# Optimization experiments

Hardware: AMD Instinct MI355X
Metric: run time of the kernel (lower is better)

## Reference

```python
import jax, jax.numpy as jnp
import numpy as np

B, P, C, H, W = 256, 512, 512, 7, 8
T = H * W  # 56
EPS = 1e-8


def setup_inputs() -> dict:
    key = jax.random.key(0)
    k1, k2, k3 = jax.random.split(key, 3)
    inp = jax.random.normal(k1, (B, C, H, W), dtype=jnp.float32)
    # xavier-uniform-like init for prototype (fan over last two dims as torch does)
    bound_p = float(np.sqrt(6.0 / (P + C * T)))
    prototype = jax.random.uniform(k2, (P, C, T), dtype=jnp.float32, minval=-bound_p, maxval=bound_p)
    bound_w = float(np.sqrt(6.0 / (C + 1)))
    fc_w = jax.random.uniform(k3, (1, C), dtype=jnp.float32, minval=-bound_w, maxval=bound_w)
    fc_b = jnp.zeros((1,), dtype=jnp.float32)
    return {"input": inp, "prototype": prototype, "fc_w": fc_w, "fc_b": fc_b}


def reference(input, prototype, fc_w, fc_b):
    # flatten spatial dims: (B, C, T)
    x = input.reshape(input.shape[0], input.shape[1], -1)
    # per-position cosine similarity over channel dim
    dots = jnp.einsum('bct,pct->bpt', x, prototype)          # (B, P, T)
    xn = jnp.linalg.norm(x, axis=1)                           # (B, T)
    pn = jnp.linalg.norm(prototype, axis=1)                   # (P, T)
    sim = dots / jnp.maximum(xn[:, None, :] * pn[None, :, :], EPS)
    att = jax.nn.softmax(sim, axis=-1)                        # (B, P, T)
    # attention-pooled elementwise product: (B, P, C)
    feat = jnp.einsum('bpt,bct,pct->bpc', att, x, prototype)
    # fc: Linear(C, 1) then relu, view to (B, P)
    out = jax.nn.relu(jnp.einsum('bpc,oc->bpo', feat, fc_w) + fc_b)
    return out.reshape(out.shape[0], out.shape[1])
```

## Files before the change

kernel.cpp:

```cpp
#include <hip/hip_runtime.h>
#include <hip/hip_bf16.h>
#include <math.h>

constexpr int kB = 256, kC = 512, kT = 56, kP = 512;
constexpr int kCT = kC * kT;

typedef short v4s __attribute__((ext_vector_type(4)));
typedef short v8s __attribute__((ext_vector_type(8)));
typedef float v4f __attribute__((ext_vector_type(4)));
typedef float v16f __attribute__((ext_vector_type(16)));

__device__ __forceinline__ unsigned pack_bf16(float a, float b) {
  __hip_bfloat16 ha = __float2bfloat16(a);
  __hip_bfloat16 hb = __float2bfloat16(b);
  unsigned short ua, ub;
  __builtin_memcpy(&ua, &ha, 2);
  __builtin_memcpy(&ub, &hb, 2);
  return (unsigned)ua | ((unsigned)ub << 16);
}

__device__ __forceinline__ v4s frag2(unsigned w0, unsigned w1) {
  unsigned u[2] = {w0, w1};
  v4s s;
  __builtin_memcpy(&s, u, 8);
  return s;
}

__device__ __forceinline__ v8s frag8(uint4 u) {
  v8s s;
  __builtin_memcpy(&s, &u, 16);
  return s;
}

__device__ __forceinline__ unsigned cvtpk(float lo, float hi) {
  unsigned r;
  asm("v_cvt_pk_bf16_f32 %0, %1, %2" : "=v"(r) : "v"(lo), "v"(hi));
  return r;
}

#define GLOAD(gp, lp)                                                        \
  __builtin_amdgcn_global_load_lds(                                          \
      (const __attribute__((address_space(1))) unsigned*)(const unsigned*)(gp), \
      (__attribute__((address_space(3))) unsigned*)(unsigned*)(lp), 16, 0, 0)

__global__ __launch_bounds__(512) void zero_kernel(float* __restrict__ p) {
  p[blockIdx.x * 512 + threadIdx.x] = 0.f;
}

__global__ __launch_bounds__(512) void prep_kernel(
    const float* __restrict__ x, const float* __restrict__ proto,
    const float* __restrict__ fcw,
    unsigned* __restrict__ xt, unsigned* __restrict__ xwt,
    unsigned* __restrict__ pt,
    float* __restrict__ xn2, float* __restrict__ pn2) {
  __shared__ float tile[128 * 64];
  __shared__ float normp[56 * 16];

  const int tid = threadIdx.x;
  const int bidx = blockIdx.x;
  const int n = bidx >> 2;
  const int ch = bidx & 3;
  const bool isx = (n < kB);
  const int row = isx ? n : (n - kB);
  const float* csrc = (isx ? x : proto) + (size_t)row * kCT + ch * (128 * 56);

  const int l = tid & 63;
  const int w = tid >> 6;
  const int j = l & 15;
  const int tq = l >> 4;

  float fw[8];
  if (isx) {
    const float* gf = fcw + ch * 128 + 8 * j;
#pragma unroll
    for (int i = 0; i < 8; ++i) fw[i] = gf[i];
  }

#pragma unroll
  for (int it = 0; it < 4; ++it) {
    const int idx = it * 512 + tid;
    if (idx < 1792) {
      const int f0 = idx * 4;
      const int c = (int)(((unsigned)f0 * 74899u) >> 22);
      const int t = f0 - c * 56;
      const int sw = ((((unsigned)c >> 3) ^ (unsigned)c) & 7) << 2;
      float4 v = *(const float4*)(csrc + f0);
      *(float4*)(tile + c * 64 + (t ^ sw)) = v;
    }
  }
  __syncthreads();

#pragma unroll
  for (int pass = 0; pass < 2; ++pass) {
    const int t = pass * 32 + w * 4 + tq;
    if (t < 56) {
      float f[8];
#pragma unroll
      for (int i = 0; i < 8; ++i) {
        const int sw = ((j ^ i) & 7) << 2;
        f[i] = tile[(8 * j + i) * 64 + (t ^ sw)];
      }
      float s = 0.f;
#pragma unroll
      for (int i = 0; i < 8; ++i) s = fmaf(f[i], f[i], s);
      normp[t * 16 + j] = s;
      uint4 wx;
      wx.x = cvtpk(f[0], f[1]);
      wx.y = cvtpk(f[2], f[3]);
      wx.z = cvtpk(f[4], f[5]);
      wx.w = cvtpk(f[6], f[7]);
      if (isx) {
        const size_t o = ((size_t)(t * kB + row)) * 256 + ch * 64 + 4 * j;
        *(uint4*)(xt + o) = wx;
        uint4 ww;
        ww.x = cvtpk(f[0] * fw[0], f[1] * fw[1]);
        ww.y = cvtpk(f[2] * fw[2], f[3] * fw[3]);
        ww.z = cvtpk(f[4] * fw[4], f[5] * fw[5]);
        ww.w = cvtpk(f[6] * fw[6], f[7] * fw[7]);
        *(uint4*)(xwt + o) = ww;
      } else {
        *(uint4*)(pt + ((size_t)(t * kP + row)) * 256 + ch * 64 + 4 * j) = wx;
      }
    }
  }
  __syncthreads();

  if (tid < 56) {
    float s = 0.f;
#pragma unroll
    for (int k = 0; k < 16; ++k) s += normp[tid * 16 + k];
    if (isx) atomicAdd(&xn2[row * 56 + tid], s);
    else     atomicAdd(&pn2[row * 56 + tid], s);
  }
}

constexpr int TILE = 64 * 32;
constexpr int BUF = 3 * TILE;

__global__ __launch_bounds__(256, 2) void proto_gemm_kernel(
    const unsigned* __restrict__ xt, const unsigned* __restrict__ xwt,
    const unsigned* __restrict__ pt,
    const float* __restrict__ xn2, const float* __restrict__ pn2,
    float* __restrict__ part) {
  __shared__ __align__(16) unsigned lds[3 * BUF];
  __shared__ float xnL[4 * 64], pnL[4 * 64];

  const int tid = threadIdx.x;
  const int l = tid & 63;
  const int w4 = tid >> 6;
  const int wm = w4 >> 1;
  const int wn = w4 & 1;

  int bid = (int)blockIdx.x;
  bid = (bid & 7) * 56 + (bid >> 3);
  const int b0 = (bid & 3) * 64;
  const int p0 = ((bid >> 2) & 7) * 64;
  const int tg = bid >> 5;

  {
    const int tl = tid >> 6, r = tid & 63;
    xnL[tid] = sqrtf(xn2[(b0 + r) * 56 + tg * 4 + tl]);
    pnL[tid] = sqrtf(pn2[(p0 + r) * 56 + tg * 4 + tl]);
  }
  __syncthreads();

  const int lrow = l >> 3, lch = l & 7;
  size_t xsrc[2], psrc[2];
  int ldst[2];
#pragma unroll
  for (int j = 0; j < 2; ++j) {
    const int row = w4 * 16 + j * 8 + lrow;
    const int ch4 = ((lch ^ (row & 7))) * 4;
    xsrc[j] = (size_t)(b0 + row) * 256 + ch4;
    psrc[j] = (size_t)(p0 + row) * 256 + ch4;
    ldst[j] = (w4 * 16 + j * 8) * 32;
  }

  const int fr = l & 31;
  const int hi = l >> 5;
  const int axb = (wm * 32 + fr) * 32;
  const int pxb = (wn * 32 + fr) * 32;
  const int frs = fr & 7;

  v16f aD, aW, sac, nac;
#pragma unroll
  for (int i = 0; i < 16; ++i) { aD[i] = 0.f; aW[i] = 0.f; sac[i] = 0.f; nac[i] = 0.f; }

  auto STAGE = [&](int s, int buf) {
    const int t = tg * 4 + (s >> 3);
    const size_t xo = (size_t)t * (kB * 256) + (size_t)((s & 7) * 32);
    const size_t po = (size_t)t * (kP * 256) + (size_t)((s & 7) * 32);
    unsigned* lb = lds + buf * BUF;
#pragma unroll
    for (int j = 0; j < 2; ++j) {
      GLOAD(xt + xsrc[j] + xo, lb + ldst[j]);
      GLOAD(xwt + xsrc[j] + xo, lb + TILE + ldst[j]);
      GLOAD(pt + psrc[j] + po, lb + 2 * TILE + ldst[j]);
    }
  };

  auto COMPUTE = [&](int s, int buf) {
    const unsigned* bx = lds + buf * BUF;
#pragma unroll
    for (int ks = 0; ks < 4; ++ks) {
      const int col = (((ks << 1) | hi) ^ frs) << 2;
      v8s xf = frag8(*(const uint4*)(bx + axb + col));
      v8s wf = frag8(*(const uint4*)(bx + TILE + axb + col));
      v8s pf = frag8(*(const uint4*)(bx + 2 * TILE + pxb + col));
      aD = __builtin_amdgcn_mfma_f32_32x32x16_bf16(xf, pf, aD, 0, 0, 0);
      aW = __builtin_amdgcn_mfma_f32_32x32x16_bf16(wf, pf, aW, 0, 0, 0);
    }
    if ((s & 7) == 7) {
      const int tl = s >> 3;
      const float pnv = pnL[tl * 64 + wn * 32 + fr];
#pragma unroll
      for (int i = 0; i < 16; ++i) {
        const int drow = (i & 3) + 8 * (i >> 2) + 4 * hi;
        const float xnv = xnL[tl * 64 + wm * 32 + drow];
        float den = fmaxf(xnv * pnv, 1e-8f);
        float sim = aD[i] * __builtin_amdgcn_rcpf(den);
        float e = __expf(sim);
        sac[i] += e;
        nac[i] = fmaf(e, aW[i], nac[i]);
        aD[i] = 0.f;
        aW[i] = 0.f;
      }
    }
  };

  STAGE(0, 0);
  STAGE(1, 1);

  int c0 = 0, c1 = 1, c2 = 2;
#pragma unroll 1
  for (int s = 0; s < 32; ++s) {
    if (s < 31) asm volatile("s_waitcnt vmcnt(6)" ::: "memory");
    else        asm volatile("s_waitcnt vmcnt(0)" ::: "memory");
    __builtin_amdgcn_s_barrier();
    __builtin_amdgcn_sched_barrier(0);
    COMPUTE(s, c0);
    if (s < 30) STAGE(s + 2, c2);
    const int tmp = c0; c0 = c1; c1 = c2; c2 = tmp;
  }

  float* psb = part + ((size_t)tg * 2 + 0) * 131072;
  float* pnb = part + ((size_t)tg * 2 + 1) * 131072;
#pragma unroll
  for (int i = 0; i < 16; ++i) {
    const int drow = (i & 3) + 8 * (i >> 2) + 4 * hi;
    const size_t o = (size_t)(b0 + wm * 32 + drow) * 512 + p0 + wn * 32 + fr;
    psb[o] = sac[i];
    pnb[o] = nac[i];
  }
}

__global__ __launch_bounds__(256) void merge_kernel(
    const float* __restrict__ part, const float* __restrict__ fcb,
    float* __restrict__ out) {
  const int pair = blockIdx.x * 256 + threadIdx.x;
  float S = 0.f, N = 0.f;
#pragma unroll
  for (int k = 0; k < 14; ++k) {
    S += part[((size_t)k * 2 + 0) * 131072 + pair];
    N += part[((size_t)k * 2 + 1) * 131072 + pair];
  }
  float o = N * __builtin_amdgcn_rcpf(S) + fcb[0];
  out[pair] = fmaxf(o, 0.f);
}

__global__ __launch_bounds__(1024) void proto_mfma_kernel(
    const float* __restrict__ x, const float* __restrict__ proto,
    const float* __restrict__ fcw, const float* __restrict__ fcb,
    float* __restrict__ out) {
  __shared__ unsigned xs[56 * 289];
  __shared__ unsigned ps[56 * 145];
  __shared__ unsigned pws[56 * 145];

  const int tid = threadIdx.x;
  const int l = tid & 63;
  const int w = tid >> 6;
  const int bq = w & 1;
  const int tq = w >> 1;
  const int t0 = tq * 7;

  const int n = blockIdx.y * 32 + blockIdx.x;
  const int p0 = (n >> 3) * 16;
  const int b0 = (n & 7) * 32;

  const bool act = (l < 56);
  const int lt = l;

  const int xbase0 = ((b0 + 2 * w + 0) * kC) * kT + lt;
  const int xbase1 = ((b0 + 2 * w + 1) * kC) * kT + lt;
  const int pbase = ((p0 + w) * kC) * kT + lt;

  const int arow = l & 15;
  const int q2 = (l >> 4) << 1;
  const int xoff = (bq * 16 + arow) * 9 + q2;
  const int poff = arow * 9 + q2;

  v4f acc[7][2];
#pragma unroll
  for (int ti = 0; ti < 7; ++ti) {
    acc[ti][0] = v4f{0.f, 0.f, 0.f, 0.f};
    acc[ti][1] = v4f{0.f, 0.f, 0.f, 0.f};
  }
  float xn2a = 0.f, xn2b = 0.f, pn2 = 0.f;

#pragma unroll 1
  for (int st = 0; st < 32; ++st) {
    const int k0 = st * 16;
    if (act) {
#pragma unroll
      for (int r = 0; r < 16; ++r) {
        const int cw = r & 7;
        const int c = k0 + 2 * cw;
        const int ga = ((r >> 3) ? xbase1 : xbase0) + c * kT;
        float g0 = x[ga], g1 = x[ga + kT];
        if (r >> 3) xn2b = fmaf(g0, g0, fmaf(g1, g1, xn2b));
        else xn2a = fmaf(g0, g0, fmaf(g1, g1, xn2a));
        xs[lt * 289 + (2 * w + (r >> 3)) * 9 + cw] = pack_bf16(g0, g1);
      }
#pragma unroll
      for (int cw = 0; cw < 8; ++cw) {
        const int c = k0 + 2 * cw;
        const int ga = pbase + c * kT;
        float g0 = proto[ga], g1 = proto[ga + kT];
        pn2 = fmaf(g0, g0, fmaf(g1, g1, pn2));
        ps[lt * 145 + w * 9 + cw] = pack_bf16(g0, g1);
        float f0 = fcw[c], f1 = fcw[c + 1];
        pws[lt * 145 + w * 9 + cw] = pack_bf16(g0 * f0, g1 * f1);
      }
    }
    __syncthreads();
#pragma unroll
    for (int ti = 0; ti < 7; ++ti) {
      const int t = t0 + ti;
      unsigned xw0 = xs[t * 289 + xoff];
      unsigned xw1 = xs[t * 289 + xoff + 1];
      unsigned pw0 = ps[t * 145 + poff];
      unsigned pw1 = ps[t * 145 + poff + 1];
      unsigned ww0 = pws[t * 145 + poff];
      unsigned ww1 = pws[t * 145 + poff + 1];
      v4s af = frag2(xw0, xw1);
      v4s bf = frag2(pw0, pw1);
      v4s wf = frag2(ww0, ww1);
      acc[ti][0] = __builtin_amdgcn_mfma_f32_16x16x16bf16_1k(af, bf, acc[ti][0], 0, 0, 0);
      acc[ti][1] = __builtin_amdgcn_mfma_f32_16x16x16bf16_1k(af, wf, acc[ti][1], 0, 0, 0);
    }
    __syncthreads();
  }

  float* xnorm = (float*)ps;
  float* pnorm = xnorm + 32 * 56;
  if (act) {
    xnorm[(2 * w + 0) * 56 + lt] = xn2a;
    xnorm[(2 * w + 1) * 56 + lt] = xn2b;
    pnorm[w * 56 + lt] = pn2;
  }
  __syncthreads();

  float* fm = (float*)xs;
  float* fsum = fm + 4096;
  float* fnum = fsum + 4096;
  const int pc = arow;
  const int qq = l >> 4;
#pragma unroll
  for (int i = 0; i < 4; ++i) {
    const int bl = bq * 16 + 4 * qq + i;
    float m = -3.0e38f;
    float sims[7];
#pragma unroll
    for (int ti = 0; ti < 7; ++ti) {
      const int t = t0 + ti;
      float den = fmaxf(sqrtf(xnorm[bl * 56 + t]) * sqrtf(pnorm[pc * 56 + t]), 1e-8f);
      float s = acc[ti][0][i] / den;
      sims[ti] = s;
      m = fmaxf(m, s);
    }
    float se = 0.f, nu = 0.f;
#pragma unroll
    for (int ti = 0; ti < 7; ++ti) {
      float e = __expf(sims[ti] - m);
      se += e;
      nu = fmaf(e, acc[ti][1][i], nu);
    }
    const int pair = bl * 16 + pc;
    fm[tq * 512 + pair] = m;
    fsum[tq * 512 + pair] = se;
    fnum[tq * 512 + pair] = nu;
  }
  __syncthreads();

  if (tid < 512) {
    float M = -3.0e38f;
#pragma unroll
    for (int k = 0; k < 8; ++k) M = fmaxf(M, fm[k * 512 + tid]);
    float S = 0.f, N = 0.f;
#pragma unroll
    for (int k = 0; k < 8; ++k) {
      float sc = __expf(fm[k * 512 + tid] - M);
      S = fmaf(fsum[k * 512 + tid], sc, S);
      N = fmaf(fnum[k * 512 + tid], sc, N);
    }
    float o = N / S + fcb[0];
    out[(b0 + (tid >> 4)) * kP + p0 + (tid & 15)] = fmaxf(o, 0.f);
  }
}

extern "C" void kernel_launch(void* const* d_in, const int* in_sizes, int n_in,
                              void* d_out, int out_size, void* d_ws, size_t ws_size,
                              hipStream_t stream) {
  const float* x = (const float*)d_in[0];
  const float* proto = (const float*)d_in[1];
  const float* fcw = (const float*)d_in[2];
  const float* fcb = (const float*)d_in[3];
  float* out = (float*)d_out;

  const size_t need = 73572352;
  if (ws_size >= need) {
    unsigned* xt = (unsigned*)d_ws;
    unsigned* xwt = xt + 3670016;
    unsigned* ptb = xt + 7340032;
    float* partb = (float*)(xt + 14680064);
    float* xn2b = (float*)(xt + 18350080);
    float* pn2b = xn2b + 14336;

    hipLaunchKernelGGL(zero_kernel, dim3(84), dim3(512), 0, stream, xn2b);

    hipLaunchKernelGGL(prep_kernel, dim3(4 * (kB + kP)), dim3(512), 0, stream,
                       x, proto, fcw, xt, xwt, ptb, xn2b, pn2b);
    hipLaunchKernelGGL(proto_gemm_kernel, dim3(448), dim3(256), 0, stream,
                       xt, xwt, ptb, xn2b, pn2b, partb);
    hipLaunchKernelGGL(merge_kernel, dim3(512), dim3(256), 0, stream,
                       partb, fcb, out);
  } else {
    hipLaunchKernelGGL(proto_mfma_kernel, dim3(32, 8), dim3(1024), 0, stream,
                       x, proto, fcw, fcb, out);
  }
}
```

Before: 67.27 us.

## Process all channel chunks per block in prep, drop zero kernel and atomics

The prep kernel now runs one block per row and loops over the four channel chunks itself. It keeps the norm partials in registers and writes the squared norms directly, so the separate zero kernel and the atomic adds are no longer needed. The bf16 staging layout changes to group four time positions per 1024-word row block, and the GEMM load addressing is updated to match. This removes one launch and the atomics, at the cost of fewer, longer-running prep blocks with less parallelism and a changed global write pattern.

```diff
diff --git a/kernel.cpp b/kernel.cpp
--- a/kernel.cpp
+++ b/kernel.cpp
@@ -43,9 +43,6 @@
       (const __attribute__((address_space(1))) unsigned*)(const unsigned*)(gp), \
       (__attribute__((address_space(3))) unsigned*)(unsigned*)(lp), 16, 0, 0)
 
-__global__ __launch_bounds__(512) void zero_kernel(float* __restrict__ p) {
-  p[blockIdx.x * 512 + threadIdx.x] = 0.f;
-}
 
 __global__ __launch_bounds__(512) void prep_kernel(
     const float* __restrict__ x, const float* __restrict__ proto,
@@ -57,80 +54,93 @@
   __shared__ float normp[56 * 16];
 
   const int tid = threadIdx.x;
-  const int bidx = blockIdx.x;
-  const int n = bidx >> 2;
-  const int ch = bidx & 3;
+  const int n = blockIdx.x;
   const bool isx = (n < kB);
   const int row = isx ? n : (n - kB);
-  const float* csrc = (isx ? x : proto) + (size_t)row * kCT + ch * (128 * 56);
+  const float* src = (isx ? x : proto) + (size_t)row * kCT;
+  const int R = isx ? kB : kP;
+  unsigned* dst0 = isx ? xt : pt;
 
   const int l = tid & 63;
   const int w = tid >> 6;
   const int j = l & 15;
   const int tq = l >> 4;
 
-  float fw[8];
-  if (isx) {
-    const float* gf = fcw + ch * 128 + 8 * j;
-#pragma unroll
-    for (int i = 0; i < 8; ++i) fw[i] = gf[i];
-  }
-
-#pragma unroll
-  for (int it = 0; it < 4; ++it) {
-    const int idx = it * 512 + tid;
-    if (idx < 1792) {
-      const int f0 = idx * 4;
-      const int c = (int)(((unsigned)f0 * 74899u) >> 22);
-      const int t = f0 - c * 56;
-      const int sw = ((((unsigned)c >> 3) ^ (unsigned)c) & 7) << 2;
-      float4 v = *(const float4*)(csrc + f0);
-      *(float4*)(tile + c * 64 + (t ^ sw)) = v;
-    }
+  float na0 = 0.f, na1 = 0.f;
+
+#pragma unroll 1
+  for (int ch = 0; ch < 4; ++ch) {
+    const float* csrc = src + ch * (128 * 56);
+
+    float fw[8];
+    if (isx) {
+      const float* gf = fcw + ch * 128 + 8 * j;
+#pragma unroll
+      for (int i = 0; i < 8; ++i) fw[i] = gf[i];
+    }
+
+#pragma unroll
+    for (int it = 0; it < 4; ++it) {
+      const int idx = it * 512 + tid;
+      if (idx < 1792) {
+        const int f0 = idx * 4;
+        const int c = (int)(((unsigned)f0 * 74899u) >> 22);
+        const int t = f0 - c * 56;
+        const int sw = ((((unsigned)c >> 3) ^ (unsigned)c) & 7) << 2;
+        float4 v = *(const float4*)(csrc + f0);
+        *(float4*)(tile + c * 64 + (t ^ sw)) = v;
+      }
+    }
+    __syncthreads();
+
+#pragma unroll
+    for (int pass = 0; pass < 2; ++pass) {
+      const int t = pass * 32 + w * 4 + tq;
+      if (t < 56) {
+        float f[8];
+#pragma unroll
+        for (int i = 0; i < 8; ++i) {
+          const int sw = ((j ^ i) & 7) << 2;
+          f[i] = tile[(8 * j + i) * 64 + (t ^ sw)];
+        }
+        float s = 0.f;
+#pragma unroll
+        for (int i = 0; i < 8; ++i) s = fmaf(f[i], f[i], s);
+        if (pass == 0) na0 += s; else na1 += s;
+        uint4 wx;
+        wx.x = cvtpk(f[0], f[1]);
+        wx.y = cvtpk(f[2], f[3]);
+        wx.z = cvtpk(f[4], f[5]);
+        wx.w = cvtpk(f[6], f[7]);
+        const size_t o = (size_t)(t >> 2) * ((size_t)R * 1024) +
+                         (size_t)row * 1024 + ch * 256 + (t & 3) * 64 + 4 * j;
+        *(uint4*)(dst0 + o) = wx;
+        if (isx) {
+          uint4 ww;
+          ww.x = cvtpk(f[0] * fw[0], f[1] * fw[1]);
+          ww.y = cvtpk(f[2] * fw[2], f[3] * fw[3]);
+          ww.z = cvtpk(f[4] * fw[4], f[5] * fw[5]);
+          ww.w = cvtpk(f[6] * fw[6], f[7] * fw[7]);
+          *(uint4*)(xwt + o) = ww;
+        }
+      }
+    }
+    __syncthreads();
+  }
+
+  {
+    const int t0 = w * 4 + tq;
+    normp[t0 * 16 + j] = na0;
+    const int t1 = 32 + w * 4 + tq;
+    if (t1 < 56) normp[t1 * 16 + j] = na1;
   }
   __syncthreads();
-
-#pragma unroll
-  for (int pass = 0; pass < 2; ++pass) {
-    const int t = pass * 32 + w * 4 + tq;
-    if (t < 56) {
-      float f[8];
-#pragma unroll
-      for (int i = 0; i < 8; ++i) {
-        const int sw = ((j ^ i) & 7) << 2;
-        f[i] = tile[(8 * j + i) * 64 + (t ^ sw)];
-      }
-      float s = 0.f;
-#pragma unroll
-      for (int i = 0; i < 8; ++i) s = fmaf(f[i], f[i], s);
-      normp[t * 16 + j] = s;
-      uint4 wx;
-      wx.x = cvtpk(f[0], f[1]);
-      wx.y = cvtpk(f[2], f[3]);
-      wx.z = cvtpk(f[4], f[5]);
-      wx.w = cvtpk(f[6], f[7]);
-      if (isx) {
-        const size_t o = ((size_t)(t * kB + row)) * 256 + ch * 64 + 4 * j;
-        *(uint4*)(xt + o) = wx;
-        uint4 ww;
-        ww.x = cvtpk(f[0] * fw[0], f[1] * fw[1]);
-        ww.y = cvtpk(f[2] * fw[2], f[3] * fw[3]);
-        ww.z = cvtpk(f[4] * fw[4], f[5] * fw[5]);
-        ww.w = cvtpk(f[6] * fw[6], f[7] * fw[7]);
-        *(uint4*)(xwt + o) = ww;
-      } else {
-        *(uint4*)(pt + ((size_t)(t * kP + row)) * 256 + ch * 64 + 4 * j) = wx;
-      }
-    }
-  }
-  __syncthreads();
-
   if (tid < 56) {
     float s = 0.f;
 #pragma unroll
     for (int k = 0; k < 16; ++k) s += normp[tid * 16 + k];
-    if (isx) atomicAdd(&xn2[row * 56 + tid], s);
-    else     atomicAdd(&pn2[row * 56 + tid], s);
+    if (isx) xn2[row * 56 + tid] = s;
+    else     pn2[row * 56 + tid] = s;
   }
 }
 
@@ -171,8 +181,8 @@
   for (int j = 0; j < 2; ++j) {
     const int row = w4 * 16 + j * 8 + lrow;
     const int ch4 = ((lch ^ (row & 7))) * 4;
-    xsrc[j] = (size_t)(b0 + row) * 256 + ch4;
-    psrc[j] = (size_t)(p0 + row) * 256 + ch4;
+    xsrc[j] = (size_t)(b0 + row) * 1024 + ch4;
+    psrc[j] = (size_t)(p0 + row) * 1024 + ch4;
     ldst[j] = (w4 * 16 + j * 8) * 32;
   }
 
@@ -188,8 +198,11 @@
 
   auto STAGE = [&](int s, int buf) {
     const int t = tg * 4 + (s >> 3);
-    const size_t xo = (size_t)t * (kB * 256) + (size_t)((s & 7) * 32);
-    const size_t po = (size_t)t * (kP * 256) + (size_t)((s & 7) * 32);
+    const int kw = s & 7;
+    const size_t base = (size_t)(t >> 2) * 1024 + (size_t)((t & 3) * 64) +
+                        (size_t)((kw >> 1) * 256 + (kw & 1) * 32);
+    const size_t xo = (size_t)(t >> 2) * ((size_t)kB * 1024 - 1024) + base;
+    const size_t po = (size_t)(t >> 2) * ((size_t)kP * 1024 - 1024) + base;
     unsigned* lb = lds + buf * BUF;
 #pragma unroll
     for (int j = 0; j < 2; ++j) {
@@ -426,9 +439,7 @@
     float* xn2b = (float*)(xt + 18350080);
     float* pn2b = xn2b + 14336;
 
-    hipLaunchKernelGGL(zero_kernel, dim3(84), dim3(512), 0, stream, xn2b);
-
-    hipLaunchKernelGGL(prep_kernel, dim3(4 * (kB + kP)), dim3(512), 0, stream,
+    hipLaunchKernelGGL(prep_kernel, dim3(kB + kP), dim3(512), 0, stream,
                        x, proto, fcw, xt, xwt, ptb, xn2b, pn2b);
     hipLaunchKernelGGL(proto_gemm_kernel, dim3(448), dim3(256), 0, stream,
                        xt, xwt, ptb, xn2b, pn2b, partb);
```

Result: faster. 61.36 us (-8.8%).
